# Kernel tuning notes

Measured on AMD Instinct MI355X. Metric: run time of the kernel, lower is better.

## Reference

```python
import jax, jax.numpy as jnp
import numpy as np

K = 20          # neighbors per centroid
OUT_CH = 256    # out_channel
EPS = 1e-5      # batchnorm eps


def _bn(x, gamma, beta, axes):
    # batch-norm in training mode (batch statistics), per-channel on last axis
    mu = jnp.mean(x, axis=axes, keepdims=True)
    var = jnp.var(x, axis=axes, keepdims=True)
    return (x - mu) * jax.lax.rsqrt(var + EPS) * gamma + beta


def _forward(centroid, xyz, radius, dist,
             w_xyz, b_xyz, g0, be0, w1, g1, be1, w2, g2, be2):
    B, N, _ = xyz.shape
    M = centroid.shape[1]
    # --- sample_and_group: radius mask + index sort + gather ---
    ar = jnp.arange(N, dtype=jnp.int32)                       # [N]
    idx = jnp.where(dist > radius, N, ar[None, None, :])      # [B,M,N]
    idx = jnp.sort(idx, axis=-1)[:, :, :K]                    # [B,M,K] lowest in-radius indices
    first = idx[:, :, :1]
    idx = jnp.where(idx == N, first, idx)                     # pad with first neighbor
    pf = jax.vmap(lambda f, i: f[i])(xyz, idx)                # [B,M,K,3] gather
    # --- concat (points, neighbors, variance) -> 9 channels ---
    pts = jnp.broadcast_to(centroid[:, :, None, :], (B, M, K, 3))
    feat = jnp.concatenate([pts, pf, pf - pts], axis=-1)      # [B,M,K,9]
    # --- 1x1 conv2d + BN2d + GELU (exact erf, as torch nn.GELU) ---
    h = jnp.einsum('bmkc,oc->bmko', feat, w_xyz) + b_xyz      # [B,M,K,C/8]
    h = jax.nn.gelu(_bn(h, g0, be0, axes=(0, 1, 2)), approximate=False)
    # --- max over k neighbors ---
    h = jnp.max(h, axis=2)                                    # [B,M,C/8]
    # --- MLP: Conv1x1 (no bias) + BN1d + GELU, then Conv1x1 + BN1d ---
    h = jnp.einsum('bmc,oc->bmo', h, w1)
    h = jax.nn.gelu(_bn(h, g1, be1, axes=(0, 1)), approximate=False)
    h = jnp.einsum('bmc,oc->bmo', h, w2)
    h = _bn(h, g2, be2, axes=(0, 1))                          # [B,M,OUT_CH]
    return h


def setup_inputs() -> dict:
    key = jax.random.key(0)
    ks = jax.random.split(key, 10)
    B, M, N = 4, 2048, 8192
    c8, c4 = OUT_CH // 8, OUT_CH // 4
    return {
        'centroid': jax.random.uniform(ks[0], (B, M, 3), jnp.float32),
        'xyz': jax.random.uniform(ks[1], (B, N, 3), jnp.float32),
        'radius': jax.random.uniform(ks[2], (B, M, 1), jnp.float32),
        'dist': jax.random.uniform(ks[3], (B, M, N), jnp.float32),
        'w_xyz': jax.random.normal(ks[4], (c8, 9), jnp.float32) * 0.3,
        'b_xyz': jnp.zeros((c8,), jnp.float32),
        'g0': jnp.ones((c8,), jnp.float32),
        'be0': jnp.zeros((c8,), jnp.float32),
        'w1': jax.random.normal(ks[5], (c4, c8), jnp.float32) * 0.2,
        'g1': jnp.ones((c4,), jnp.float32),
        'be1': jnp.zeros((c4,), jnp.float32),
        'w2': jax.random.normal(ks[6], (OUT_CH, c4), jnp.float32) * 0.15,
        'g2': jnp.ones((OUT_CH,), jnp.float32),
        'be2': jnp.zeros((OUT_CH,), jnp.float32),
    }


def reference(centroid, xyz, radius, dist, w_xyz, b_xyz, g0, be0,
              w1, g1, be1, w2, g2, be2):
    return _forward(centroid, xyz, radius, dist, w_xyz, b_xyz, g0, be0,
                    w1, g1, be1, w2, g2, be2)
```

## Files before the change

kernel.cpp:

```cpp
#include <hip/hip_runtime.h>
#include <cstdint>
#include <cstddef>

#define K_NB   20
#define N_PTS  8192
#define C8     32
#define C4     64
#define COUT   256
#define EPSV   1e-5f
#define NROWS  8192
#define NBLK   512
#define RPW    4
#define NP0    16
#define NP1    16
#define NP2    16

__device__ __forceinline__ float gelu_exact(float x) {
    return 0.5f * x * (1.0f + erff(x * 0.7071067811865476f));
}

__device__ __forceinline__ void grid_barrier(unsigned* __restrict__ arrive,
                                             unsigned* __restrict__ release,
                                             unsigned tag) {
    __syncthreads();
    if (blockIdx.x == 0) {
        for (int i = threadIdx.x; i < NBLK; i += 256) {
            if (i != 0)
                while (__hip_atomic_load(&arrive[i], __ATOMIC_ACQUIRE,
                                         __HIP_MEMORY_SCOPE_AGENT) != tag)
                    __builtin_amdgcn_s_sleep(2);
        }
        __syncthreads();
        if (threadIdx.x == 0)
            __hip_atomic_store(&release[tag], tag, __ATOMIC_RELEASE,
                               __HIP_MEMORY_SCOPE_AGENT);
    } else {
        if (threadIdx.x == 0) {
            __hip_atomic_store(&arrive[blockIdx.x], tag, __ATOMIC_RELEASE,
                               __HIP_MEMORY_SCOPE_AGENT);
            while (__hip_atomic_load(&release[tag], __ATOMIC_ACQUIRE,
                                     __HIP_MEMORY_SCOPE_AGENT) != tag)
                __builtin_amdgcn_s_sleep(2);
        }
        __syncthreads();
    }
}

__device__ __forceinline__ double agent_load(const double* p) {
    return __hip_atomic_load(p, __ATOMIC_RELAXED, __HIP_MEMORY_SCOPE_AGENT);
}

__global__ __launch_bounds__(256, 4) void k_fused(
    const float* __restrict__ centroid, const float* __restrict__ xyz,
    const float* __restrict__ radius,   const float* __restrict__ dist,
    const float* __restrict__ w_xyz,    const float* __restrict__ b_xyz,
    const float* __restrict__ g0,  const float* __restrict__ be0,
    const float* __restrict__ w1,  const float* __restrict__ g1,
    const float* __restrict__ be1, const float* __restrict__ w2,
    const float* __restrict__ g2,  const float* __restrict__ be2,
    float* __restrict__ out,
    double* __restrict__ p0sum, double* __restrict__ p0sq,
    double* __restrict__ p1sum, double* __restrict__ p1sq,
    double* __restrict__ p2sum, double* __restrict__ p2sq,
    unsigned* __restrict__ barr_arrive, unsigned* __restrict__ barr_release)
{
    __shared__ int   idx_sh[4][K_NB];
    __shared__ float ss[256], qq[256];
    __shared__ float sc0[C8],  sh0[C8];
    __shared__ float w1t[C8 * C4];
    __shared__ float a_sh[4][RPW][C8];
    __shared__ float sc1[C4],  sh1[C4];
    __shared__ float a1_sh[4][RPW][C4];
    __shared__ float s2s[4][COUT], q2s[4][COUT];
    __shared__ float sc2[COUT], sh2[COUT];

    const int tid  = threadIdx.x;
    const int wave = tid >> 6;
    const int lane = tid & 63;
    const int gw   = blockIdx.x * 4 + wave;
    const int ch   = lane & 31;
    const int kk   = lane >> 5;

    const float* wr = w_xyz + ch * 9;
    const float wc0 = wr[0] - wr[6], wc1 = wr[1] - wr[7], wc2 = wr[2] - wr[8];
    const float wp0 = wr[3] + wr[6], wp1 = wr[4] + wr[7], wp2 = wr[5] + wr[8];
    const float bch = b_xyz[ch];

    float e[RPW];
    float s_acc = 0.f, q_acc = 0.f;

    for (int r = 0; r < RPW; ++r) {
        const int row = gw * RPW + r;
        const int b   = row >> 11;
        const float rad = radius[row];
        const float* drow = dist + (size_t)row * N_PTS;

        int cnt = 0;
        for (int base = 0; base < N_PTS && cnt < K_NB; base += 1024) {
            float4 v[4];
            #pragma unroll
            for (int s = 0; s < 4; s++)
                v[s] = reinterpret_cast<const float4*>(drow + base + s * 256)[lane];
            #pragma unroll
            for (int s = 0; s < 4; s++) {
                unsigned mloc = (v[s].x <= rad ? 1u : 0u) | (v[s].y <= rad ? 2u : 0u)
                              | (v[s].z <= rad ? 4u : 0u) | (v[s].w <= rad ? 8u : 0u);
                uint64_t b0 = __ballot(mloc & 1u);
                uint64_t b1 = __ballot(mloc & 2u);
                uint64_t b2 = __ballot(mloc & 4u);
                uint64_t b3 = __ballot(mloc & 8u);
                uint64_t lt = (1ull << lane) - 1ull;
                int rk = __popcll(b0 & lt) + __popcll(b1 & lt)
                       + __popcll(b2 & lt) + __popcll(b3 & lt);
                const int myidx = base + s * 256 + lane * 4;
                if (mloc & 1u) { int p = cnt + rk; if (p < K_NB) idx_sh[wave][p] = myidx + 0; rk++; }
                if (mloc & 2u) { int p = cnt + rk; if (p < K_NB) idx_sh[wave][p] = myidx + 1; rk++; }
                if (mloc & 4u) { int p = cnt + rk; if (p < K_NB) idx_sh[wave][p] = myidx + 2; rk++; }
                if (mloc & 8u) { int p = cnt + rk; if (p < K_NB) idx_sh[wave][p] = myidx + 3; rk++; }
                cnt += __popcll(b0) + __popcll(b1) + __popcll(b2) + __popcll(b3);
            }
        }
        __syncthreads();
        const int cfill = (cnt < K_NB) ? cnt : K_NB;
        const int fillv = (cnt == 0) ? (N_PTS - 1) : idx_sh[wave][0];
        if (lane < K_NB && lane >= cfill) idx_sh[wave][lane] = fillv;
        __syncthreads();

        const float cterm = bch + centroid[row * 3 + 0] * wc0
                          + centroid[row * 3 + 1] * wc1
                          + centroid[row * 3 + 2] * wc2;
        float s = 0.f, q = 0.f, mn = 3.0e38f, mx = -3.0e38f;
        #pragma unroll
        for (int t = 0; t < 10; t++) {
            const int idx = idx_sh[wave][2 * t + kk];
            const float* p = xyz + ((size_t)b * N_PTS + idx) * 3;
            const float h = cterm + p[0] * wp0 + p[1] * wp1 + p[2] * wp2;
            s += h; q += h * h;
            mn = fminf(mn, h); mx = fmaxf(mx, h);
        }
        s_acc += s; q_acc += q;
        mn = fminf(mn, __shfl_xor(mn, 32));
        mx = fmaxf(mx, __shfl_xor(mx, 32));
        e[r] = (lane < 32) ? mn : mx;
    }

    ss[tid] = s_acc; qq[tid] = q_acc;
    __syncthreads();
    if (tid < C8) {
        float S = 0.f, Q = 0.f;
        #pragma unroll
        for (int rr = 0; rr < 8; rr++) { S += ss[tid + 32 * rr]; Q += qq[tid + 32 * rr]; }
        const int part = blockIdx.x & (NP0 - 1);
        atomicAdd(&p0sum[part * C8 + tid], (double)S);
        atomicAdd(&p0sq [part * C8 + tid], (double)Q);
    }
    grid_barrier(barr_arrive, barr_release, 1u);

    if (tid < C8) {
        double S = 0.0, Q = 0.0;
        #pragma unroll 8
        for (int p = 0; p < NP0; p++) { S += agent_load(&p0sum[p * C8 + tid]);
                                        Q += agent_load(&p0sq [p * C8 + tid]); }
        const double inv = 1.0 / (double)((long)NROWS * K_NB);
        const double mu  = S * inv;
        const double var = Q * inv - mu * mu;
        const float sf = g0[tid] / sqrtf((float)var + EPSV);
        sc0[tid] = sf;
        sh0[tid] = be0[tid] - (float)mu * sf;
    }
    for (int i = tid; i < C4 * C8; i += 256) {
        const int o = i >> 5, c = i & 31;
        w1t[c * C4 + o] = w1[i];
    }
    __syncthreads();

    #pragma unroll
    for (int r = 0; r < RPW; ++r) {
        float g = gelu_exact(e[r] * sc0[ch] + sh0[ch]);
        g = fmaxf(g, __shfl_xor(g, 32));
        if (lane < 32) a_sh[wave][r][lane] = g;
    }
    __syncthreads();

    float h1r[RPW];
    #pragma unroll
    for (int r = 0; r < RPW; ++r) {
        float acc = 0.f;
        #pragma unroll
        for (int c = 0; c < C8; c++) acc += a_sh[wave][r][c] * w1t[c * C4 + lane];
        h1r[r] = acc;
    }
    {
        float S = 0.f, Q = 0.f;
        #pragma unroll
        for (int r = 0; r < RPW; ++r) { S += h1r[r]; Q += h1r[r] * h1r[r]; }
        ss[tid] = S; qq[tid] = Q;
    }
    __syncthreads();
    if (tid < C4) {
        const float S = ss[tid] + ss[tid + 64] + ss[tid + 128] + ss[tid + 192];
        const float Q = qq[tid] + qq[tid + 64] + qq[tid + 128] + qq[tid + 192];
        const int part = blockIdx.x & (NP1 - 1);
        atomicAdd(&p1sum[part * C4 + tid], (double)S);
        atomicAdd(&p1sq [part * C4 + tid], (double)Q);
    }
    grid_barrier(barr_arrive, barr_release, 2u);

    if (tid < C4) {
        double S = 0.0, Q = 0.0;
        #pragma unroll 8
        for (int p = 0; p < NP1; p++) { S += agent_load(&p1sum[p * C4 + tid]);
                                        Q += agent_load(&p1sq [p * C4 + tid]); }
        const double inv = 1.0 / (double)NROWS;
        const double mu  = S * inv;
        const double var = Q * inv - mu * mu;
        const float sf = g1[tid] / sqrtf((float)var + EPSV);
        sc1[tid] = sf;
        sh1[tid] = be1[tid] - (float)mu * sf;
    }
    __syncthreads();
    #pragma unroll
    for (int r = 0; r < RPW; ++r)
        a1_sh[wave][r][lane] = gelu_exact(h1r[r] * sc1[lane] + sh1[lane]);
    __syncthreads();

    float acc[RPW][4] = {};
    #pragma unroll 4
    for (int c = 0; c < C4; ++c) {
        float av[RPW];
        #pragma unroll
        for (int r = 0; r < RPW; ++r) av[r] = a1_sh[wave][r][c];
        #pragma unroll
        for (int j = 0; j < 4; j++) {
            const float wv = w2[(j * 64 + lane) * C4 + c];
            #pragma unroll
            for (int r = 0; r < RPW; ++r) acc[r][j] += av[r] * wv;
        }
    }
    #pragma unroll
    for (int j = 0; j < 4; j++) {
        float S = 0.f, Q = 0.f;
        #pragma unroll
        for (int r = 0; r < RPW; ++r) { S += acc[r][j]; Q += acc[r][j] * acc[r][j]; }
        s2s[wave][j * 64 + lane] = S;
        q2s[wave][j * 64 + lane] = Q;
    }
    __syncthreads();
    {
        const float S = s2s[0][tid] + s2s[1][tid] + s2s[2][tid] + s2s[3][tid];
        const float Q = q2s[0][tid] + q2s[1][tid] + q2s[2][tid] + q2s[3][tid];
        const int part = blockIdx.x & (NP2 - 1);
        atomicAdd(&p2sum[part * COUT + tid], (double)S);
        atomicAdd(&p2sq [part * COUT + tid], (double)Q);
    }
    grid_barrier(barr_arrive, barr_release, 3u);

    {
        double S = 0.0, Q = 0.0;
        #pragma unroll 8
        for (int p = 0; p < NP2; p++) { S += agent_load(&p2sum[p * COUT + tid]);
                                        Q += agent_load(&p2sq [p * COUT + tid]); }
        const double inv = 1.0 / (double)NROWS;
        const double mu  = S * inv;
        const double var = Q * inv - mu * mu;
        const float sf = g2[tid] / sqrtf((float)var + EPSV);
        sc2[tid] = sf;
        sh2[tid] = be2[tid] - (float)mu * sf;
    }
    __syncthreads();
    #pragma unroll
    for (int r = 0; r < RPW; ++r) {
        const int row = gw * RPW + r;
        float* orow = out + (size_t)row * COUT;
        #pragma unroll
        for (int j = 0; j < 4; j++) {
            const int oc = j * 64 + lane;
            orow[oc] = acc[r][j] * sc2[oc] + sh2[oc];
        }
    }
}

extern "C" void kernel_launch(void* const* d_in, const int* in_sizes, int n_in,
                              void* d_out, int out_size, void* d_ws, size_t ws_size,
                              hipStream_t stream) {
    const float* centroid = (const float*)d_in[0];
    const float* xyz      = (const float*)d_in[1];
    const float* radius   = (const float*)d_in[2];
    const float* dist     = (const float*)d_in[3];
    const float* w_xyz    = (const float*)d_in[4];
    const float* b_xyz    = (const float*)d_in[5];
    const float* g0       = (const float*)d_in[6];
    const float* be0      = (const float*)d_in[7];
    const float* w1       = (const float*)d_in[8];
    const float* g1       = (const float*)d_in[9];
    const float* be1      = (const float*)d_in[10];
    const float* w2       = (const float*)d_in[11];
    const float* g2       = (const float*)d_in[12];
    const float* be2      = (const float*)d_in[13];
    float* out = (float*)d_out;

    char* ws = (char*)d_ws;
    double* p0sum = (double*)ws;
    double* p0sq  = p0sum + NP0 * C8;
    double* p1sum = p0sq  + NP0 * C8;
    double* p1sq  = p1sum + NP1 * C4;
    double* p2sum = p1sq  + NP1 * C4;
    double* p2sq  = p2sum + NP2 * COUT;
    unsigned* barr_arrive  = (unsigned*)(ws + 131072);
    unsigned* barr_release = (unsigned*)(ws + 131072 + 4096);

    k_fused<<<NBLK, 256, 0, stream>>>(centroid, xyz, radius, dist,
                                      w_xyz, b_xyz, g0, be0, w1, g1, be1,
                                      w2, g2, be2, out,
                                      p0sum, p0sq, p1sum, p1sq, p2sum, p2sq,
                                      barr_arrive, barr_release);
}
```

Before: 508.5 us.

## Double grid size, overlap two rows' distance scans, trim intra-block syncs

The grid doubles to 1024 blocks, each wave now handling 2 rows instead of 4, and the partial-statistics slices grow to 32 to match. Each wave issues the first distance chunk for both of its rows before processing either, so the two loads overlap. Several __syncthreads are dropped where the shared data is private to one wave, the w1 transpose is moved ahead of the first grid barrier, the barrier polling uses relaxed loads with a shorter sleep, and w2 is read as float4. The aim is more memory-level parallelism in the latency-bound dist scan and less synchronization. The risk is that the persistent grid barrier now needs all 1024 blocks resident at once, and relaxed polling weakens the memory ordering the barrier relies on.

Result: faster. 437.8 us (-13.9%).

```diff
diff --git a/kernel.cpp b/kernel.cpp
--- a/kernel.cpp
+++ b/kernel.cpp
@@ -9,11 +9,11 @@
 #define COUT   256
 #define EPSV   1e-5f
 #define NROWS  8192
-#define NBLK   512
-#define RPW    4
-#define NP0    16
-#define NP1    16
-#define NP2    16
+#define NBLK   1024
+#define RPW    2
+#define NP0    32
+#define NP1    32
+#define NP2    32
 
 __device__ __forceinline__ float gelu_exact(float x) {
     return 0.5f * x * (1.0f + erff(x * 0.7071067811865476f));
@@ -26,9 +26,9 @@
     if (blockIdx.x == 0) {
         for (int i = threadIdx.x; i < NBLK; i += 256) {
             if (i != 0)
-                while (__hip_atomic_load(&arrive[i], __ATOMIC_ACQUIRE,
+                while (__hip_atomic_load(&arrive[i], __ATOMIC_RELAXED,
                                          __HIP_MEMORY_SCOPE_AGENT) != tag)
-                    __builtin_amdgcn_s_sleep(2);
+                    __builtin_amdgcn_s_sleep(1);
         }
         __syncthreads();
         if (threadIdx.x == 0)
@@ -38,9 +38,9 @@
         if (threadIdx.x == 0) {
             __hip_atomic_store(&arrive[blockIdx.x], tag, __ATOMIC_RELEASE,
                                __HIP_MEMORY_SCOPE_AGENT);
-            while (__hip_atomic_load(&release[tag], __ATOMIC_ACQUIRE,
+            while (__hip_atomic_load(&release[tag], __ATOMIC_RELAXED,
                                      __HIP_MEMORY_SCOPE_AGENT) != tag)
-                __builtin_amdgcn_s_sleep(2);
+                __builtin_amdgcn_s_sleep(1);
         }
         __syncthreads();
     }
@@ -48,6 +48,29 @@
 
 __device__ __forceinline__ double agent_load(const double* p) {
     return __hip_atomic_load(p, __ATOMIC_RELAXED, __HIP_MEMORY_SCOPE_AGENT);
+}
+
+__device__ __forceinline__ int chunk_process(const float4* v, float rad, int base,
+                                             int lane, int* __restrict__ idxp, int cnt) {
+    #pragma unroll
+    for (int s = 0; s < 4; s++) {
+        unsigned mloc = (v[s].x <= rad ? 1u : 0u) | (v[s].y <= rad ? 2u : 0u)
+                      | (v[s].z <= rad ? 4u : 0u) | (v[s].w <= rad ? 8u : 0u);
+        uint64_t b0 = __ballot(mloc & 1u);
+        uint64_t b1 = __ballot(mloc & 2u);
+        uint64_t b2 = __ballot(mloc & 4u);
+        uint64_t b3 = __ballot(mloc & 8u);
+        uint64_t lt = (1ull << lane) - 1ull;
+        int r = __popcll(b0 & lt) + __popcll(b1 & lt)
+              + __popcll(b2 & lt) + __popcll(b3 & lt);
+        const int myidx = base + s * 256 + lane * 4;
+        if (mloc & 1u) { int p = cnt + r; if (p < K_NB) idxp[p] = myidx + 0; r++; }
+        if (mloc & 2u) { int p = cnt + r; if (p < K_NB) idxp[p] = myidx + 1; r++; }
+        if (mloc & 4u) { int p = cnt + r; if (p < K_NB) idxp[p] = myidx + 2; r++; }
+        if (mloc & 8u) { int p = cnt + r; if (p < K_NB) idxp[p] = myidx + 3; r++; }
+        cnt += __popcll(b0) + __popcll(b1) + __popcll(b2) + __popcll(b3);
+    }
+    return cnt;
 }
 
 __global__ __launch_bounds__(256, 4) void k_fused(
@@ -64,7 +87,7 @@
     double* __restrict__ p2sum, double* __restrict__ p2sq,
     unsigned* __restrict__ barr_arrive, unsigned* __restrict__ barr_release)
 {
-    __shared__ int   idx_sh[4][K_NB];
+    __shared__ int   idx_sh[4][RPW][K_NB];
     __shared__ float ss[256], qq[256];
     __shared__ float sc0[C8],  sh0[C8];
     __shared__ float w1t[C8 * C4];
@@ -78,6 +101,8 @@
     const int wave = tid >> 6;
     const int lane = tid & 63;
     const int gw   = blockIdx.x * 4 + wave;
+    const int row0 = gw * RPW;
+    const int b    = row0 >> 11;
     const int ch   = lane & 31;
     const int kk   = lane >> 5;
 
@@ -86,53 +111,57 @@
     const float wp0 = wr[3] + wr[6], wp1 = wr[4] + wr[7], wp2 = wr[5] + wr[8];
     const float bch = b_xyz[ch];
 
+    const float rad0 = radius[row0];
+    const float rad1 = radius[row0 + 1];
+    const float* d0 = dist + (size_t)row0 * N_PTS;
+    const float* d1 = d0 + N_PTS;
+    int* idx0 = idx_sh[wave][0];
+    int* idx1 = idx_sh[wave][1];
+
+    float4 va[4], vb[4];
+    #pragma unroll
+    for (int s = 0; s < 4; s++) va[s] = reinterpret_cast<const float4*>(d0 + s * 256)[lane];
+    #pragma unroll
+    for (int s = 0; s < 4; s++) vb[s] = reinterpret_cast<const float4*>(d1 + s * 256)[lane];
+    int cnt0 = chunk_process(va, rad0, 0, lane, idx0, 0);
+    int cnt1 = chunk_process(vb, rad1, 0, lane, idx1, 0);
+    for (int base = 1024; base < N_PTS && cnt0 < K_NB; base += 1024) {
+        #pragma unroll
+        for (int s = 0; s < 4; s++)
+            va[s] = reinterpret_cast<const float4*>(d0 + base + s * 256)[lane];
+        cnt0 = chunk_process(va, rad0, base, lane, idx0, cnt0);
+    }
+    for (int base = 1024; base < N_PTS && cnt1 < K_NB; base += 1024) {
+        #pragma unroll
+        for (int s = 0; s < 4; s++)
+            vb[s] = reinterpret_cast<const float4*>(d1 + base + s * 256)[lane];
+        cnt1 = chunk_process(vb, rad1, base, lane, idx1, cnt1);
+    }
+
+    {
+        const int cf = (cnt0 < K_NB) ? cnt0 : K_NB;
+        const int fv = (cnt0 == 0) ? (N_PTS - 1) : idx0[0];
+        if (lane < K_NB && lane >= cf) idx0[lane] = fv;
+    }
+    {
+        const int cf = (cnt1 < K_NB) ? cnt1 : K_NB;
+        const int fv = (cnt1 == 0) ? (N_PTS - 1) : idx1[0];
+        if (lane < K_NB && lane >= cf) idx1[lane] = fv;
+    }
+
     float e[RPW];
     float s_acc = 0.f, q_acc = 0.f;
-
+    #pragma unroll
     for (int r = 0; r < RPW; ++r) {
-        const int row = gw * RPW + r;
-        const int b   = row >> 11;
-        const float rad = radius[row];
-        const float* drow = dist + (size_t)row * N_PTS;
-
-        int cnt = 0;
-        for (int base = 0; base < N_PTS && cnt < K_NB; base += 1024) {
-            float4 v[4];
-            #pragma unroll
-            for (int s = 0; s < 4; s++)
-                v[s] = reinterpret_cast<const float4*>(drow + base + s * 256)[lane];
-            #pragma unroll
-            for (int s = 0; s < 4; s++) {
-                unsigned mloc = (v[s].x <= rad ? 1u : 0u) | (v[s].y <= rad ? 2u : 0u)
-                              | (v[s].z <= rad ? 4u : 0u) | (v[s].w <= rad ? 8u : 0u);
-                uint64_t b0 = __ballot(mloc & 1u);
-                uint64_t b1 = __ballot(mloc & 2u);
-                uint64_t b2 = __ballot(mloc & 4u);
-                uint64_t b3 = __ballot(mloc & 8u);
-                uint64_t lt = (1ull << lane) - 1ull;
-                int rk = __popcll(b0 & lt) + __popcll(b1 & lt)
-                       + __popcll(b2 & lt) + __popcll(b3 & lt);
-                const int myidx = base + s * 256 + lane * 4;
-                if (mloc & 1u) { int p = cnt + rk; if (p < K_NB) idx_sh[wave][p] = myidx + 0; rk++; }
-                if (mloc & 2u) { int p = cnt + rk; if (p < K_NB) idx_sh[wave][p] = myidx + 1; rk++; }
-                if (mloc & 4u) { int p = cnt + rk; if (p < K_NB) idx_sh[wave][p] = myidx + 2; rk++; }
-                if (mloc & 8u) { int p = cnt + rk; if (p < K_NB) idx_sh[wave][p] = myidx + 3; rk++; }
-                cnt += __popcll(b0) + __popcll(b1) + __popcll(b2) + __popcll(b3);
-            }
-        }
-        __syncthreads();
-        const int cfill = (cnt < K_NB) ? cnt : K_NB;
-        const int fillv = (cnt == 0) ? (N_PTS - 1) : idx_sh[wave][0];
-        if (lane < K_NB && lane >= cfill) idx_sh[wave][lane] = fillv;
-        __syncthreads();
-
+        const int row = row0 + r;
         const float cterm = bch + centroid[row * 3 + 0] * wc0
                           + centroid[row * 3 + 1] * wc1
                           + centroid[row * 3 + 2] * wc2;
+        const int* idxp = idx_sh[wave][r];
         float s = 0.f, q = 0.f, mn = 3.0e38f, mx = -3.0e38f;
         #pragma unroll
         for (int t = 0; t < 10; t++) {
-            const int idx = idx_sh[wave][2 * t + kk];
+            const int idx = idxp[2 * t + kk];
             const float* p = xyz + ((size_t)b * N_PTS + idx) * 3;
             const float h = cterm + p[0] * wp0 + p[1] * wp1 + p[2] * wp2;
             s += h; q += h * h;
@@ -142,6 +171,11 @@
         mn = fminf(mn, __shfl_xor(mn, 32));
         mx = fmaxf(mx, __shfl_xor(mx, 32));
         e[r] = (lane < 32) ? mn : mx;
+    }
+
+    for (int i = tid; i < C4 * C8; i += 256) {
+        const int o = i >> 5, c = i & 31;
+        w1t[c * C4 + o] = w1[i];
     }
 
     ss[tid] = s_acc; qq[tid] = q_acc;
@@ -168,21 +202,15 @@
         sc0[tid] = sf;
         sh0[tid] = be0[tid] - (float)mu * sf;
     }
-    for (int i = tid; i < C4 * C8; i += 256) {
-        const int o = i >> 5, c = i & 31;
-        w1t[c * C4 + o] = w1[i];
-    }
-    __syncthreads();
-
+    __syncthreads();
+
+    float h1r[RPW];
     #pragma unroll
     for (int r = 0; r < RPW; ++r) {
         float g = gelu_exact(e[r] * sc0[ch] + sh0[ch]);
         g = fmaxf(g, __shfl_xor(g, 32));
         if (lane < 32) a_sh[wave][r][lane] = g;
     }
-    __syncthreads();
-
-    float h1r[RPW];
     #pragma unroll
     for (int r = 0; r < RPW; ++r) {
         float acc = 0.f;
@@ -190,12 +218,8 @@
         for (int c = 0; c < C8; c++) acc += a_sh[wave][r][c] * w1t[c * C4 + lane];
         h1r[r] = acc;
     }
-    {
-        float S = 0.f, Q = 0.f;
-        #pragma unroll
-        for (int r = 0; r < RPW; ++r) { S += h1r[r]; Q += h1r[r] * h1r[r]; }
-        ss[tid] = S; qq[tid] = Q;
-    }
+    ss[tid] = h1r[0] + h1r[1];
+    qq[tid] = h1r[0] * h1r[0] + h1r[1] * h1r[1];
     __syncthreads();
     if (tid < C4) {
         const float S = ss[tid] + ss[tid + 64] + ss[tid + 128] + ss[tid + 192];
@@ -222,19 +246,22 @@
     #pragma unroll
     for (int r = 0; r < RPW; ++r)
         a1_sh[wave][r][lane] = gelu_exact(h1r[r] * sc1[lane] + sh1[lane]);
-    __syncthreads();
-
+
+    const float4* w2v = reinterpret_cast<const float4*>(w2);
     float acc[RPW][4] = {};
-    #pragma unroll 4
-    for (int c = 0; c < C4; ++c) {
-        float av[RPW];
-        #pragma unroll
-        for (int r = 0; r < RPW; ++r) av[r] = a1_sh[wave][r][c];
-        #pragma unroll
-        for (int j = 0; j < 4; j++) {
-            const float wv = w2[(j * 64 + lane) * C4 + c];
+    #pragma unroll
+    for (int j = 0; j < 4; j++) {
+        const int o = j * 64 + lane;
+        #pragma unroll
+        for (int c4 = 0; c4 < 16; c4++) {
+            const float4 wv = w2v[o * 16 + c4];
             #pragma unroll
-            for (int r = 0; r < RPW; ++r) acc[r][j] += av[r] * wv;
+            for (int r = 0; r < RPW; r++) {
+                acc[r][j] += a1_sh[wave][r][4 * c4 + 0] * wv.x
+                           + a1_sh[wave][r][4 * c4 + 1] * wv.y
+                           + a1_sh[wave][r][4 * c4 + 2] * wv.z
+                           + a1_sh[wave][r][4 * c4 + 3] * wv.w;
+            }
         }
     }
     #pragma unroll
@@ -270,8 +297,7 @@
     __syncthreads();
     #pragma unroll
     for (int r = 0; r < RPW; ++r) {
-        const int row = gw * RPW + r;
-        float* orow = out + (size_t)row * COUT;
+        float* orow = out + (size_t)(row0 + r) * COUT;
         #pragma unroll
         for (int j = 0; j < 4; j++) {
             const int oc = j * 64 + lane;
@@ -306,8 +332,8 @@
     double* p1sq  = p1sum + NP1 * C4;
     double* p2sum = p1sq  + NP1 * C4;
     double* p2sq  = p2sum + NP2 * COUT;
-    unsigned* barr_arrive  = (unsigned*)(ws + 131072);
-    unsigned* barr_release = (unsigned*)(ws + 131072 + 4096);
+    unsigned* barr_arrive  = (unsigned*)(ws + 262144);
+    unsigned* barr_release = (unsigned*)(ws + 262144 + 8192);
 
     k_fused<<<NBLK, 256, 0, stream>>>(centroid, xyz, radius, dist,
                                       w_xyz, b_xyz, g0, be0, w1, g1, be1,
```
